# Performance work log

Measured on AMD Instinct MI355X. Metric: run time of the kernel, lower is better.

Reference implementation:

```python
import jax, jax.numpy as jnp
import numpy as np

IN_FEATURES = 8192
OUT_FEATURES = 8192
CODESZ = 8            # E8 lattice dimension per code index
CODEBOOK_SIZE = 65536 # 2^16-entry codebook (16-bit indices)
TOKENS = 32           # decode-style batch


def fwht(x):
    """Fast Walsh-Hadamard transform (Sylvester order) along the last axis.
    n must be a power of 2. Unnormalized (multiply by H_n)."""
    n = x.shape[-1]
    steps = int(np.log2(n))
    h = 1
    for _ in range(steps):
        y = x.reshape(*x.shape[:-1], n // (2 * h), 2, h)
        a = y[..., 0, :]
        b = y[..., 1, :]
        x = jnp.stack([a + b, a - b], axis=-2).reshape(*y.shape[:-3], n)
        h *= 2
    return x


def setup_inputs() -> dict:
    key = jax.random.key(0)
    k0, k1, k2, k3, k4 = jax.random.split(key, 5)
    x = jax.random.normal(k0, (TOKENS, IN_FEATURES), dtype=jnp.float32)
    # learned codebook: CODEBOOK_SIZE vectors of CODESZ entries (E8P-like lattice points)
    codebook_table = jax.random.normal(k1, (CODEBOOK_SIZE, CODESZ), dtype=jnp.float32) * 0.1
    # quantized weight indices: [out_features, in_features // codesz]
    Qidxs = jax.random.randint(k2, (OUT_FEATURES, IN_FEATURES // CODESZ), 0, CODEBOOK_SIZE, dtype=jnp.int32)
    # random sign vectors (incoherence processing)
    SU = (2.0 * jax.random.randint(k3, (IN_FEATURES,), 0, 2) - 1.0).astype(jnp.float32)
    SV = (2.0 * jax.random.randint(k4, (OUT_FEATURES,), 0, 2) - 1.0).astype(jnp.float32)
    Wscale = jnp.array(0.02, dtype=jnp.float32)
    return {"x": x, "codebook_table": codebook_table, "Qidxs": Qidxs,
            "SU": SU, "SV": SV, "Wscale": Wscale}


def reference(x, codebook_table, Qidxs, SU, SV, Wscale):
    n_in = x.shape[-1]
    n_out = SV.shape[0]
    # input incoherence: sign flip then orthonormal Hadamard rotation (matmul_hadUt)
    xh = fwht(x * SU) * (1.0 / jnp.sqrt(jnp.float32(n_in)))  # [T, n_in]
    # codebook dequantization: gather lattice vectors and lay out as [n_out, n_in]
    W = codebook_table[Qidxs].reshape(n_out, n_in)
    # quantized matmul in the rotated basis
    z = xh @ W.T  # [T, n_out]
    # output rotation (matmul_hadU) + sign/scale (SV absorbs Wscale in the torch code)
    out = fwht(z) * (1.0 / jnp.sqrt(jnp.float32(n_out))) * (SV * Wscale)
    return out
```

## Files before the change

kernel.cpp:

```cpp
#include <hip/hip_runtime.h>
#include <hip/hip_bf16.h>


typedef __attribute__((ext_vector_type(16))) float f32x16;
typedef __attribute__((ext_vector_type(8))) __bf16 bf16x8;
typedef __attribute__((ext_vector_type(4))) __bf16 bf16x4;
typedef __attribute__((ext_vector_type(4))) int i32x4;

#define IN_F 8192
#define OUT_F 8192
#define TOKENS 32
#define KSPLIT 8
#define KCHUNK 1024
#define CH (KCHUNK / 8)
#define GROUPS (KCHUNK / 32)
#define DG 5
#define DI 7
#define INV_SQRT_8192 0.011048543456039806f
#define PAD(i) ((i) + ((i) >> 5))

#if __has_builtin(__builtin_amdgcn_raw_buffer_load_b128) && \
    __has_builtin(__builtin_amdgcn_make_buffer_rsrc)
#define HAVE_BUF 1
#else
#define HAVE_BUF 0
#endif

__device__ inline void fwht32_reg(float* r) {
    #pragma unroll
    for (int h = 1; h < 32; h <<= 1)
        #pragma unroll
        for (int i = 0; i < 32; i += 2 * h)
            #pragma unroll
            for (int j = 0; j < h; ++j) {
                float a = r[i + j], b = r[i + j + h];
                r[i + j] = a + b;
                r[i + j + h] = a - b;
            }
}

__device__ inline void fwht8192_lds(float* s, int tid) {
    float r[32];
    int b1 = tid * 32;
    #pragma unroll
    for (int j = 0; j < 32; ++j) r[j] = s[PAD(b1 + j)];
    fwht32_reg(r);
    #pragma unroll
    for (int j = 0; j < 32; ++j) s[PAD(b1 + j)] = r[j];
    __syncthreads();
    int b2 = (tid & 31) + (tid >> 5) * 1024;
    #pragma unroll
    for (int j = 0; j < 32; ++j) r[j] = s[PAD(b2 + 32 * j)];
    fwht32_reg(r);
    #pragma unroll
    for (int j = 0; j < 32; ++j) s[PAD(b2 + 32 * j)] = r[j];
    __syncthreads();
    #pragma unroll
    for (int jj = 0; jj < 4; ++jj) {
        float g[8];
        int b3 = tid * 4 + jj;
        #pragma unroll
        for (int k = 0; k < 8; ++k) g[k] = s[PAD(b3 + 1024 * k)];
        #pragma unroll
        for (int h = 1; h < 8; h <<= 1)
            #pragma unroll
            for (int i = 0; i < 8; i += 2 * h)
                #pragma unroll
                for (int j = 0; j < h; ++j) {
                    float a = g[i + j], b = g[i + j + h];
                    g[i + j] = a + b;
                    g[i + j + h] = a - b;
                }
        #pragma unroll
        for (int k = 0; k < 8; ++k) s[PAD(b3 + 1024 * k)] = g[k];
    }
    __syncthreads();
}

__global__ __launch_bounds__(256)
void prep_kernel(const float* __restrict__ cb, __bf16* __restrict__ cbb,
                 const float* __restrict__ x, const float* __restrict__ su,
                 __bf16* __restrict__ xh) {
    __shared__ float s[8192 + 256];
    const int tid = threadIdx.x;
    if (blockIdx.x < 512) {
        int i = blockIdx.x * 256 + tid;
        float4 v = ((const float4*)cb)[i];
        bf16x4 o;
        o[0] = (__bf16)v.x; o[1] = (__bf16)v.y;
        o[2] = (__bf16)v.z; o[3] = (__bf16)v.w;
        ((bf16x4*)cbb)[i] = o;
        return;
    }
    const int t = blockIdx.x - 512;
    #pragma unroll
    for (int i = tid; i < IN_F; i += 256)
        s[PAD(i)] = x[t * IN_F + i] * su[i];
    __syncthreads();
    fwht8192_lds(s, tid);
    #pragma unroll
    for (int i = tid; i < IN_F; i += 256)
        xh[t * IN_F + i] = (__bf16)(s[PAD(i)] * INV_SQRT_8192);
}

__global__ __launch_bounds__(512, 4)
void qgemm_kernel(const int* __restrict__ qidxs,
                  const __bf16* __restrict__ cb,
                  const __bf16* __restrict__ xh,
                  __bf16* __restrict__ zpart) {
    __shared__ __align__(16) __bf16 xt[TOKENS * KCHUNK];
    const int ks = blockIdx.x & (KSPLIT - 1);
    const int nb = blockIdx.x >> 3;
    const int tid = threadIdx.x;
    const int wave = tid >> 6, lane = tid & 63;
    const int h = lane >> 5, lc = lane & 31;
    const int n = nb * 256 + wave * 32 + lc;

    #pragma unroll
    for (int i = 0; i < 8; ++i) {
        int f = i * 512 + tid, r = f >> 7, c = f & 127;
        i32x4 v = *(const i32x4*)(xh + (size_t)r * IN_F + ks * KCHUNK + c * 8);
        *(i32x4*)(xt + ((r * CH + (c ^ (r & 7))) << 3)) = v;
    }
    __syncthreads();

    const int* qrow = qidxs + (size_t)n * (IN_F / 8) + ks * (KCHUNK / 8);

#if HAVE_BUF
    __amdgpu_buffer_rsrc_t rsrc = __builtin_amdgcn_make_buffer_rsrc(
        (void*)cb, (short)0, 65536 * 16, 0x00020000);
    #define GA(ix, au) __builtin_bit_cast(bf16x8, \
        __builtin_amdgcn_raw_buffer_load_b128(rsrc, (ix) << 4, 0, au))
#else
    const bf16x8* cbv = (const bf16x8*)cb;
    #define GA(ix, au) (cbv[ix])
#endif

    f32x16 acc;
    #pragma unroll
    for (int i = 0; i < 16; ++i) acc[i] = 0.f;

    i32x4 iv[GROUPS];
    bf16x8 bfr[GROUPS][2];

    #pragma unroll
    for (int g = 0; g < DI; ++g)
        iv[g] = *(const i32x4*)(qrow + g * 4);
    #pragma unroll
    for (int g = 0; g < DG; ++g) {
        if (g & 1) {
            bfr[g][0] = GA(h ? iv[g][1] : iv[g][0], 1);
            bfr[g][1] = GA(h ? iv[g][3] : iv[g][2], 1);
        } else {
            bfr[g][0] = GA(h ? iv[g][1] : iv[g][0], 0);
            bfr[g][1] = GA(h ? iv[g][3] : iv[g][2], 0);
        }
    }

    #pragma unroll
    for (int g = 0; g < GROUPS; ++g) {
        if (g + DI < GROUPS)
            iv[g + DI] = *(const i32x4*)(qrow + (g + DI) * 4);
        if (g + DG < GROUPS) {
            if ((g + DG) & 1) {
                bfr[g + DG][0] = GA(h ? iv[g + DG][1] : iv[g + DG][0], 1);
                bfr[g + DG][1] = GA(h ? iv[g + DG][3] : iv[g + DG][2], 1);
            } else {
                bfr[g + DG][0] = GA(h ? iv[g + DG][1] : iv[g + DG][0], 0);
                bfr[g + DG][1] = GA(h ? iv[g + DG][3] : iv[g + DG][2], 0);
            }
        }
        #pragma unroll
        for (int sgi = 0; sgi < 2; ++sgi) {
            const int T = 2 * g + sgi;
            bf16x8 a = *(const bf16x8*)(xt +
                          ((lc * CH + ((2 * T + h) ^ (lc & 7))) << 3));
            acc = __builtin_amdgcn_mfma_f32_32x32x16_bf16(a, bfr[g][sgi],
                                                          acc, 0, 0, 0);
        }
    }

    __bf16* zp = zpart + ((size_t)ks * TOKENS) * OUT_F + n;
    #pragma unroll
    for (int r = 0; r < 16; ++r) {
        int m = (r & 3) + 4 * h + 8 * (r >> 2);
        zp[(size_t)m * OUT_F] = (__bf16)acc[r];
    }
}

__global__ __launch_bounds__(256)
void zsum_kernel(const __bf16* __restrict__ zpart, const float* __restrict__ sv,
                 const float* __restrict__ wscale, float* __restrict__ out) {
    __shared__ float s[8192 + 256];
    const int t = blockIdx.x, tid = threadIdx.x;
    #pragma unroll
    for (int cc = 0; cc < 4; ++cc) {
        int col = cc * 2048 + tid * 8;
        float a[8] = {0.f, 0.f, 0.f, 0.f, 0.f, 0.f, 0.f, 0.f};
        #pragma unroll
        for (int ks = 0; ks < KSPLIT; ++ks) {
            bf16x8 v = *(const bf16x8*)(zpart +
                         ((size_t)(ks * TOKENS + t)) * OUT_F + col);
            #pragma unroll
            for (int j = 0; j < 8; ++j) a[j] += (float)v[j];
        }
        #pragma unroll
        for (int j = 0; j < 8; ++j) s[PAD(col + j)] = a[j];
    }
    __syncthreads();
    fwht8192_lds(s, tid);
    const float sc = INV_SQRT_8192 * wscale[0];
    #pragma unroll
    for (int i = tid; i < OUT_F; i += 256)
        out[t * OUT_F + i] = s[PAD(i)] * sc * sv[i];
}

extern "C" void kernel_launch(void* const* d_in, const int* in_sizes, int n_in,
                              void* d_out, int out_size, void* d_ws, size_t ws_size,
                              hipStream_t stream) {
    const float* x      = (const float*)d_in[0];
    const float* cb     = (const float*)d_in[1];
    const int*   qidxs  = (const int*)d_in[2];
    const float* su     = (const float*)d_in[3];
    const float* sv     = (const float*)d_in[4];
    const float* wscale = (const float*)d_in[5];
    float* out = (float*)d_out;

    char* ws = (char*)d_ws;
    __bf16* cb_bf16 = (__bf16*)ws;
    __bf16* xh      = (__bf16*)(ws + (1u << 20));
    __bf16* zpart   = (__bf16*)(ws + (1u << 20) + (512u << 10));

    hipLaunchKernelGGL(prep_kernel, dim3(544), dim3(256), 0, stream,
                       cb, cb_bf16, x, su, xh);
    hipLaunchKernelGGL(qgemm_kernel, dim3(32 * KSPLIT), dim3(512), 0, stream,
                       qidxs, cb_bf16, xh, zpart);
    hipLaunchKernelGGL(zsum_kernel, dim3(TOKENS), dim3(256), 0, stream,
                       zpart, sv, wscale, out);
}
```

Baseline: 133.9 us.

## Stage qidx rows through double-buffered LDS with coalesced loads, halve xt tile

Code indices used to be read per lane straight from each lane's own row in global memory. Now each wave loads them cooperatively in coalesced 16-byte chunks into a per-wave, double-buffered, swizzled LDS buffer, and the MFMA loop reads them back from LDS. The activation tile in LDS is halved to 512 columns and restaged halfway through the K loop, which keeps total shared memory usage unchanged. The aim is better global access efficiency for the index stream, at the cost of two extra block-wide barriers mid-loop and more complex scheduling.

```diff
diff --git a/kernel.cpp b/kernel.cpp
--- a/kernel.cpp
+++ b/kernel.cpp
@@ -12,7 +12,8 @@
 #define TOKENS 32
 #define KSPLIT 8
 #define KCHUNK 1024
-#define CH (KCHUNK / 8)
+#define XTK 512
+#define CH (XTK / 8)
 #define GROUPS (KCHUNK / 32)
 #define DG 5
 #define DI 7
@@ -108,23 +109,45 @@
                   const __bf16* __restrict__ cb,
                   const __bf16* __restrict__ xh,
                   __bf16* __restrict__ zpart) {
-    __shared__ __align__(16) __bf16 xt[TOKENS * KCHUNK];
+    __shared__ __align__(16) __bf16 xt[TOKENS * XTK];
+    __shared__ __align__(16) int qs[2][8][512];
     const int ks = blockIdx.x & (KSPLIT - 1);
     const int nb = blockIdx.x >> 3;
     const int tid = threadIdx.x;
     const int wave = tid >> 6, lane = tid & 63;
     const int h = lane >> 5, lc = lane & 31;
-    const int n = nb * 256 + wave * 32 + lc;
-
-    #pragma unroll
-    for (int i = 0; i < 8; ++i) {
-        int f = i * 512 + tid, r = f >> 7, c = f & 127;
-        i32x4 v = *(const i32x4*)(xh + (size_t)r * IN_F + ks * KCHUNK + c * 8);
-        *(i32x4*)(xt + ((r * CH + (c ^ (r & 7))) << 3)) = v;
-    }
-    __syncthreads();
-
-    const int* qrow = qidxs + (size_t)n * (IN_F / 8) + ks * (KCHUNK / 8);
+    const int n0 = nb * 256 + wave * 32;
+    const int n = n0 + lc;
+
+    auto stage_xt = [&](int h2) {
+        #pragma unroll
+        for (int i = 0; i < 4; ++i) {
+            int f = i * 512 + tid, r = f >> 6, c = f & 63;
+            i32x4 v = *(const i32x4*)(xh + (size_t)r * IN_F +
+                                      ks * KCHUNK + h2 * XTK + c * 8);
+            *(i32x4*)(xt + ((r * CH + (c ^ (r & 7))) << 3)) = v;
+        }
+    };
+
+    auto LOADC = [&](int c, i32x4* lv) {
+        #pragma unroll
+        for (int i = 0; i < 2; ++i) {
+            int slot = i * 64 + lane, row = slot >> 2, sp = slot & 3;
+            lv[i] = *(const i32x4*)(qidxs + (size_t)(n0 + row) * (IN_F / 8)
+                                    + ks * (KCHUNK / 8) + c * 16 + sp * 4);
+        }
+    };
+    auto WRITEC = [&](int c, const i32x4* lv) {
+        __builtin_amdgcn_sched_barrier(0);
+        #pragma unroll
+        for (int i = 0; i < 2; ++i) {
+            int slot = i * 64 + lane, row = slot >> 2, sp = slot & 3;
+            *(i32x4*)&qs[c & 1][wave][row * 16 + ((sp ^ (row & 3)) << 2)] =
+                lv[i];
+        }
+    };
+    #define IVRD(g) (*(const i32x4*)&qs[((g) >> 2) & 1][wave] \
+                        [lc * 16 + ((((g) & 3) ^ (lc & 3)) << 2)])
 
 #if HAVE_BUF
     __amdgpu_buffer_rsrc_t rsrc = __builtin_amdgcn_make_buffer_rsrc(
@@ -136,6 +159,13 @@
     #define GA(ix, au) (cbv[ix])
 #endif
 
+    i32x4 rA[2], rB[2];
+    LOADC(0, rA); LOADC(1, rB);
+    stage_xt(0);
+    WRITEC(0, rA); WRITEC(1, rB);
+    __syncthreads();
+    LOADC(2, rA); LOADC(3, rB);
+
     f32x16 acc;
     #pragma unroll
     for (int i = 0; i < 16; ++i) acc[i] = 0.f;
@@ -145,7 +175,7 @@
 
     #pragma unroll
     for (int g = 0; g < DI; ++g)
-        iv[g] = *(const i32x4*)(qrow + g * 4);
+        iv[g] = IVRD(g);
     #pragma unroll
     for (int g = 0; g < DG; ++g) {
         if (g & 1) {
@@ -156,11 +186,23 @@
             bfr[g][1] = GA(h ? iv[g][3] : iv[g][2], 0);
         }
     }
+    WRITEC(2, rA);
+    LOADC(4, rA);
 
     #pragma unroll
     for (int g = 0; g < GROUPS; ++g) {
+        if ((g & 3) == 1 && g <= 17) {
+            const int c = (g >> 2) + 3;
+            if (c & 1) { WRITEC(c, rB); if (c + 2 <= 7) LOADC(c + 2, rB); }
+            else       { WRITEC(c, rA); if (c + 2 <= 7) LOADC(c + 2, rA); }
+        }
+        if (g == 16) {
+            __syncthreads();
+            stage_xt(1);
+            __syncthreads();
+        }
         if (g + DI < GROUPS)
-            iv[g + DI] = *(const i32x4*)(qrow + (g + DI) * 4);
+            iv[g + DI] = IVRD(g + DI);
         if (g + DG < GROUPS) {
             if ((g + DG) & 1) {
                 bfr[g + DG][0] = GA(h ? iv[g + DG][1] : iv[g + DG][0], 1);
@@ -172,7 +214,7 @@
         }
         #pragma unroll
         for (int sgi = 0; sgi < 2; ++sgi) {
-            const int T = 2 * g + sgi;
+            const int T = 2 * (g & 15) + sgi;
             bf16x8 a = *(const bf16x8*)(xt +
                           ((lc * CH + ((2 * T + h) ^ (lc & 7))) << 3));
             acc = __builtin_amdgcn_mfma_f32_32x32x16_bf16(a, bfr[g][sgi],
```

After: 137.7 us. +2.8%, slower.

## Split 8192-point Hadamard transforms into two passes for more parallel blocks

Applied to the files above, without the earlier changes.

Each 8192-point FWHT, on the input and on the output, is now split into an 8-point register pass across strided columns and a 1024-point LDS pass done per 1024-element chunk. This replaces the old one-block-per-token kernels (only 32 blocks) with many more blocks: 128 plus 256 for the input side, 256 plus 128 for the output side. The goal is to fill the GPU for the transform stages and shorten the serial tail around the GEMM. In exchange it adds two kernel launches and extra fp32 global round trips through new workspace buffers.

```diff
diff --git a/kernel.cpp b/kernel.cpp
--- a/kernel.cpp
+++ b/kernel.cpp
@@ -26,81 +26,81 @@
 #define HAVE_BUF 0
 #endif
 
-__device__ inline void fwht32_reg(float* r) {
-    #pragma unroll
-    for (int h = 1; h < 32; h <<= 1)
-        #pragma unroll
-        for (int i = 0; i < 32; i += 2 * h)
+__device__ inline void fwht8_reg(float* v) {
+    #pragma unroll
+    for (int h = 1; h < 8; h <<= 1)
+        #pragma unroll
+        for (int i = 0; i < 8; i += 2 * h)
             #pragma unroll
             for (int j = 0; j < h; ++j) {
-                float a = r[i + j], b = r[i + j + h];
-                r[i + j] = a + b;
-                r[i + j + h] = a - b;
+                float a = v[i + j], b = v[i + j + h];
+                v[i + j] = a + b;
+                v[i + j + h] = a - b;
             }
 }
 
-__device__ inline void fwht8192_lds(float* s, int tid) {
-    float r[32];
-    int b1 = tid * 32;
-    #pragma unroll
-    for (int j = 0; j < 32; ++j) r[j] = s[PAD(b1 + j)];
-    fwht32_reg(r);
-    #pragma unroll
-    for (int j = 0; j < 32; ++j) s[PAD(b1 + j)] = r[j];
-    __syncthreads();
-    int b2 = (tid & 31) + (tid >> 5) * 1024;
-    #pragma unroll
-    for (int j = 0; j < 32; ++j) r[j] = s[PAD(b2 + 32 * j)];
-    fwht32_reg(r);
-    #pragma unroll
-    for (int j = 0; j < 32; ++j) s[PAD(b2 + 32 * j)] = r[j];
-    __syncthreads();
-    #pragma unroll
-    for (int jj = 0; jj < 4; ++jj) {
-        float g[8];
-        int b3 = tid * 4 + jj;
-        #pragma unroll
-        for (int k = 0; k < 8; ++k) g[k] = s[PAD(b3 + 1024 * k)];
-        #pragma unroll
-        for (int h = 1; h < 8; h <<= 1)
-            #pragma unroll
-            for (int i = 0; i < 8; i += 2 * h)
-                #pragma unroll
-                for (int j = 0; j < h; ++j) {
-                    float a = g[i + j], b = g[i + j + h];
-                    g[i + j] = a + b;
-                    g[i + j + h] = a - b;
-                }
-        #pragma unroll
-        for (int k = 0; k < 8; ++k) s[PAD(b3 + 1024 * k)] = g[k];
-    }
-    __syncthreads();
-}
-
-__global__ __launch_bounds__(256)
-void prep_kernel(const float* __restrict__ cb, __bf16* __restrict__ cbb,
-                 const float* __restrict__ x, const float* __restrict__ su,
-                 __bf16* __restrict__ xh) {
-    __shared__ float s[8192 + 256];
+__device__ inline void fwht1024(float v[4], float* st, int tid) {
+    {
+        float t0 = v[0] + v[1], t1 = v[0] - v[1];
+        float t2 = v[2] + v[3], t3 = v[2] - v[3];
+        v[0] = t0 + t2; v[1] = t1 + t3; v[2] = t0 - t2; v[3] = t1 - t3;
+    }
+    int pos[4] = {4 * tid, 4 * tid + 1, 4 * tid + 2, 4 * tid + 3};
+    #pragma unroll
+    for (int s = 1; s < 5; ++s) {
+        #pragma unroll
+        for (int j = 0; j < 4; ++j) st[PAD(pos[j])] = v[j];
+        __syncthreads();
+        const int q = 1 << (2 * s);
+        const int i = ((tid >> (2 * s)) << (2 * s + 2)) + (tid & (q - 1));
+        #pragma unroll
+        for (int j = 0; j < 4; ++j) { pos[j] = i + j * q; v[j] = st[PAD(pos[j])]; }
+        __syncthreads();
+        float t0 = v[0] + v[1], t1 = v[0] - v[1];
+        float t2 = v[2] + v[3], t3 = v[2] - v[3];
+        v[0] = t0 + t2; v[1] = t1 + t3; v[2] = t0 - t2; v[3] = t1 - t3;
+    }
+}
+
+__global__ __launch_bounds__(256)
+void prepA_kernel(const float* __restrict__ x, const float* __restrict__ su,
+                  float* __restrict__ xw) {
+    const int id = blockIdx.x * 256 + threadIdx.x;
+    const int t = id >> 10, c = id & 1023;
+    float v[8];
+    #pragma unroll
+    for (int k = 0; k < 8; ++k)
+        v[k] = x[t * IN_F + k * 1024 + c] * su[k * 1024 + c];
+    fwht8_reg(v);
+    #pragma unroll
+    for (int k = 0; k < 8; ++k)
+        xw[t * IN_F + k * 1024 + c] = v[k];
+}
+
+__global__ __launch_bounds__(256)
+void prepB_kernel(const float* __restrict__ cb, __bf16* __restrict__ cbb,
+                  const float* __restrict__ xw, __bf16* __restrict__ xh) {
+    __shared__ float st[1056];
     const int tid = threadIdx.x;
     if (blockIdx.x < 512) {
         int i = blockIdx.x * 256 + tid;
-        float4 v = ((const float4*)cb)[i];
+        float4 vv = ((const float4*)cb)[i];
         bf16x4 o;
-        o[0] = (__bf16)v.x; o[1] = (__bf16)v.y;
-        o[2] = (__bf16)v.z; o[3] = (__bf16)v.w;
+        o[0] = (__bf16)vv.x; o[1] = (__bf16)vv.y;
+        o[2] = (__bf16)vv.z; o[3] = (__bf16)vv.w;
         ((bf16x4*)cbb)[i] = o;
         return;
     }
-    const int t = blockIdx.x - 512;
-    #pragma unroll
-    for (int i = tid; i < IN_F; i += 256)
-        s[PAD(i)] = x[t * IN_F + i] * su[i];
-    __syncthreads();
-    fwht8192_lds(s, tid);
-    #pragma unroll
-    for (int i = tid; i < IN_F; i += 256)
-        xh[t * IN_F + i] = (__bf16)(s[PAD(i)] * INV_SQRT_8192);
+    const int id = blockIdx.x - 512;
+    const int t = id >> 3, ch = id & 7;
+    const float* src = xw + (size_t)t * IN_F + ch * 1024;
+    float4 f = ((const float4*)src)[tid];
+    float v[4] = {f.x, f.y, f.z, f.w};
+    fwht1024(v, st, tid);
+    __bf16* dst = xh + (size_t)t * IN_F + ch * 1024;
+    #pragma unroll
+    for (int j = 0; j < 4; ++j)
+        dst[tid + j * 256] = (__bf16)(v[j] * INV_SQRT_8192);
 }
 
 __global__ __launch_bounds__(512, 4)
@@ -189,30 +189,39 @@
 }
 
 __global__ __launch_bounds__(256)
-void zsum_kernel(const __bf16* __restrict__ zpart, const float* __restrict__ sv,
-                 const float* __restrict__ wscale, float* __restrict__ out) {
-    __shared__ float s[8192 + 256];
-    const int t = blockIdx.x, tid = threadIdx.x;
-    #pragma unroll
-    for (int cc = 0; cc < 4; ++cc) {
-        int col = cc * 2048 + tid * 8;
-        float a[8] = {0.f, 0.f, 0.f, 0.f, 0.f, 0.f, 0.f, 0.f};
-        #pragma unroll
-        for (int ks = 0; ks < KSPLIT; ++ks) {
-            bf16x8 v = *(const bf16x8*)(zpart +
-                         ((size_t)(ks * TOKENS + t)) * OUT_F + col);
-            #pragma unroll
-            for (int j = 0; j < 8; ++j) a[j] += (float)v[j];
-        }
-        #pragma unroll
-        for (int j = 0; j < 8; ++j) s[PAD(col + j)] = a[j];
-    }
-    __syncthreads();
-    fwht8192_lds(s, tid);
+void zsumA_kernel(const __bf16* __restrict__ zpart, float* __restrict__ z1) {
+    __shared__ float st[1056];
+    const int tid = threadIdx.x;
+    const int t = blockIdx.x >> 3, ch = blockIdx.x & 7;
+    float v[4] = {0.f, 0.f, 0.f, 0.f};
+    #pragma unroll
+    for (int ks = 0; ks < KSPLIT; ++ks) {
+        bf16x4 b = *(const bf16x4*)(zpart +
+                     ((size_t)(ks * TOKENS + t)) * OUT_F + ch * 1024 + tid * 4);
+        v[0] += (float)b[0]; v[1] += (float)b[1];
+        v[2] += (float)b[2]; v[3] += (float)b[3];
+    }
+    fwht1024(v, st, tid);
+    float* dst = z1 + (size_t)t * OUT_F + ch * 1024;
+    #pragma unroll
+    for (int j = 0; j < 4; ++j)
+        dst[tid + j * 256] = v[j];
+}
+
+__global__ __launch_bounds__(256)
+void zsumB_kernel(const float* __restrict__ z1, const float* __restrict__ sv,
+                  const float* __restrict__ wscale, float* __restrict__ out) {
+    const int id = blockIdx.x * 256 + threadIdx.x;
+    const int t = id >> 10, c = id & 1023;
+    float v[8];
+    #pragma unroll
+    for (int k = 0; k < 8; ++k)
+        v[k] = z1[t * OUT_F + k * 1024 + c];
+    fwht8_reg(v);
     const float sc = INV_SQRT_8192 * wscale[0];
     #pragma unroll
-    for (int i = tid; i < OUT_F; i += 256)
-        out[t * OUT_F + i] = s[PAD(i)] * sc * sv[i];
+    for (int k = 0; k < 8; ++k)
+        out[t * OUT_F + k * 1024 + c] = v[k] * sc * sv[k * 1024 + c];
 }
 
 extern "C" void kernel_launch(void* const* d_in, const int* in_sizes, int n_in,
@@ -230,11 +239,17 @@
     __bf16* cb_bf16 = (__bf16*)ws;
     __bf16* xh      = (__bf16*)(ws + (1u << 20));
     __bf16* zpart   = (__bf16*)(ws + (1u << 20) + (512u << 10));
-
-    hipLaunchKernelGGL(prep_kernel, dim3(544), dim3(256), 0, stream,
-                       cb, cb_bf16, x, su, xh);
+    float*  xw      = (float*)(ws + (5u << 20) + (512u << 10));
+    float*  z1      = (float*)(ws + (6u << 20) + (512u << 10));
+
+    hipLaunchKernelGGL(prepA_kernel, dim3(128), dim3(256), 0, stream,
+                       x, su, xw);
+    hipLaunchKernelGGL(prepB_kernel, dim3(768), dim3(256), 0, stream,
+                       cb, cb_bf16, xw, xh);
     hipLaunchKernelGGL(qgemm_kernel, dim3(32 * KSPLIT), dim3(512), 0, stream,
                        qidxs, cb_bf16, xh, zpart);
-    hipLaunchKernelGGL(zsum_kernel, dim3(TOKENS), dim3(256), 0, stream,
-                       zpart, sv, wscale, out);
-}
+    hipLaunchKernelGGL(zsumA_kernel, dim3(256), dim3(256), 0, stream,
+                       zpart, z1);
+    hipLaunchKernelGGL(zsumB_kernel, dim3(128), dim3(256), 0, stream,
+                       z1, sv, wscale, out);
+}
```

Result: faster. 127.8 us (-4.6%).
